# Kernel optimization log

Measured on AMD Instinct MI355X. Metric: run time of the kernel, lower is better.

The kernel has to match this reference:

```python
import jax, jax.numpy as jnp
import numpy as np

B, T, D = 64, 1024, 512      # batch, listener time, 2*listener_hidden
H = 512                      # speller_hidden_dim
M = 256                      # mlp_dim_in_attention
C = 63                       # output_class_dim
S = 64                       # max_label_len (decode steps)
INV_SQRT_2PI = 0.3989422804014327


def setup_inputs() -> dict:
    key = jax.random.key(0)
    ks = jax.random.split(key, 16)
    def lin(k, out_d, in_d, scale=1.0):
        return jax.random.normal(k, (out_d, in_d), jnp.float32) * (scale / np.sqrt(in_d))
    listener_feature = jax.random.normal(ks[0], (B, T, D), jnp.float32)
    labels = jax.random.randint(ks[1], (B, S), 0, C)
    ground_truth = jax.nn.one_hot(labels, C, dtype=jnp.float32)
    return {
        'listener_feature': listener_feature,
        'ground_truth': ground_truth,
        'phi_w': lin(ks[2], M, D, 0.5), 'phi_b': jnp.zeros((M,), jnp.float32),
        'psi_w': lin(ks[3], M, D, 0.5), 'psi_b': jnp.zeros((M,), jnp.float32),
        'w_ih0': lin(ks[4], 4 * H, C + H), 'w_hh0': lin(ks[5], 4 * H, H),
        'b_ih0': jnp.zeros((4 * H,), jnp.float32), 'b_hh0': jnp.zeros((4 * H,), jnp.float32),
        'w_ih1': lin(ks[6], 4 * H, H), 'w_hh1': lin(ks[7], 4 * H, H),
        'b_ih1': jnp.zeros((4 * H,), jnp.float32), 'b_hh1': jnp.zeros((4 * H,), jnp.float32),
        'char_w': lin(ks[8], C, 2 * H), 'char_b': jnp.zeros((C,), jnp.float32),
    }


def _lstm_cell(x, h, c, w_ih, w_hh, b_ih, b_hh):
    g = x @ w_ih.T + b_ih + h @ w_hh.T + b_hh
    i, f, gg, o = jnp.split(g, 4, axis=-1)  # torch gate order i,f,g,o
    c_new = jax.nn.sigmoid(f) * c + jax.nn.sigmoid(i) * jnp.tanh(gg)
    h_new = jax.nn.sigmoid(o) * jnp.tanh(c_new)
    return h_new, c_new


def _copula_score(energy):
    # energy: [B, T]. Gaussian marginal pdf * bivariate Gaussian copula density of
    # adjacent columns (columns 0 and T-1 keep copula factor 1, as in source loop).
    pdf = jnp.exp(-0.5 * energy * energy) * INV_SQRT_2PI
    a = energy[:, :-2]   # column i-1 for i in 1..T-2
    b = energy[:, 1:-1]  # column i
    am = a - a.mean(axis=0)
    bm = b - b.mean(axis=0)
    r = (am * bm).sum(axis=0) / jnp.sqrt((am * am).sum(axis=0) * (bm * bm).sum(axis=0) + 1e-12)
    det = 1.0 - r * r  # det of 2x2 correlation matrix
    det_s = jnp.maximum(det, 1e-6)
    quad = r * r * (a * a + b * b) - 2.0 * r * a * b
    cop = jnp.exp(-0.5 * quad / det_s) / jnp.sqrt(det_s)
    bad = (det < 0.01) | jnp.all(a == b, axis=0)
    cop = jnp.where(bad, 10.0, cop)
    coppdf = jnp.ones_like(energy).at[:, 1:-1].set(cop)
    ef1 = pdf * coppdf
    # source falls back to softmax(energy) if any column is all-zero (batch>3 here);
    # copula path goes through numpy in torch, i.e. it is detached from autograd.
    any_zero_col = jnp.any(jnp.all(energy == 0.0, axis=0))
    return jnp.where(any_zero_col,
                     jax.nn.softmax(energy, axis=-1),
                     jax.nn.softmax(jax.lax.stop_gradient(ef1), axis=-1))


def _speller(listener_feature, ground_truth, phi_w, phi_b, psi_w, psi_b,
             w_ih0, w_hh0, b_ih0, b_hh0, w_ih1, w_hh1, b_ih1, b_hh1,
             char_w, char_b):
    comp_listener = jax.nn.relu(jnp.einsum('btd,md->btm', listener_feature, psi_w) + psi_b)

    def step(carry, gt_t):
        h0, c0, h1, c1, rnn_in = carry
        h0, c0 = _lstm_cell(rnn_in, h0, c0, w_ih0, w_hh0, b_ih0, b_hh0)
        h1, c1 = _lstm_cell(h0, h1, c1, w_ih1, w_hh1, b_ih1, b_hh1)
        dec = h1  # [B, H] top-layer rnn_output
        comp_dec = jax.nn.relu(dec @ phi_w.T + phi_b)            # [B, M]
        energy = jnp.einsum('bm,btm->bt', comp_dec, comp_listener)
        att = _copula_score(energy)                              # [B, T]
        context = jnp.einsum('bt,btd->bd', att, listener_feature)
        concat = jnp.concatenate([dec, context], axis=-1)        # [B, 2H]
        raw_pred = jax.nn.log_softmax(concat @ char_w.T + char_b, axis=-1)
        new_in = jnp.concatenate([gt_t, context], axis=-1)       # teacher forcing
        return (h0, c0, h1, c1, new_in), (raw_pred, att)

    z = jnp.zeros((B, H), listener_feature.dtype)
    onehot0 = jnp.zeros((B, C), listener_feature.dtype).at[:, 0].set(1.0)
    init_in = jnp.concatenate([onehot0, listener_feature[:, 0, :]], axis=-1)
    gt_seq = jnp.transpose(ground_truth, (1, 0, 2))  # [S, B, C]
    _, (preds, atts) = jax.lax.scan(step, (z, z, z, z, init_in), gt_seq)
    return preds, atts  # [S,B,C] log-probs, [S,B,T] attention scores


def reference(listener_feature, ground_truth, phi_w, phi_b, psi_w, psi_b,
              w_ih0, w_hh0, b_ih0, b_hh0, w_ih1, w_hh1, b_ih1, b_hh1,
              char_w, char_b):
    return _speller(listener_feature, ground_truth, phi_w, phi_b, psi_w, psi_b,
                    w_ih0, w_hh0, b_ih0, b_hh0, w_ih1, w_hh1, b_ih1, b_hh1,
                    char_w, char_b)
```

## Files before the change

### kernel.cpp

```cpp
#include <hip/hip_runtime.h>
#include <hip/hip_bf16.h>
#include <math.h>

#define B_ 64
#define T_ 1024
#define D_ 512
#define H_ 512
#define M_ 256
#define CC 63
#define SS 64
#define INV_SQRT_2PI 0.3989422804014327f

typedef __attribute__((ext_vector_type(8))) short short8v;
typedef __attribute__((ext_vector_type(4))) float f32x4;

static __device__ __forceinline__ float bf2f(unsigned short u) {
    unsigned int x = ((unsigned int)u) << 16;
    return __uint_as_float(x);
}
static __device__ __forceinline__ unsigned short f2bf(float f) {
    unsigned int x = __float_as_uint(f);
    unsigned int r = (x + 0x7fff + ((x >> 16) & 1)) >> 16;
    return (unsigned short)r;
}
static __device__ __forceinline__ float sigm(float x) {
    return 1.f / (1.f + __expf(-x));
}
static __device__ __forceinline__ float wsum64(float v) {
    for (int o = 32; o > 0; o >>= 1) v += __shfl_xor(v, o, 64);
    return v;
}


__global__ __launch_bounds__(256) void k_conv(const float* __restrict__ src,
        unsigned short* __restrict__ dst, int n4) {
    int stride = gridDim.x * 256;
    for (int i = blockIdx.x * 256 + threadIdx.x; i < n4; i += stride) {
        float4 v = ((const float4*)src)[i];
        ushort4 o;
        o.x = f2bf(v.x); o.y = f2bf(v.y); o.z = f2bf(v.z); o.w = f2bf(v.w);
        ((ushort4*)dst)[i] = o;
    }
}

__global__ __launch_bounds__(256) void k_gemm_mfma(
        const unsigned short* __restrict__ Abf,
        const unsigned short* __restrict__ Bbf,
        const float* __restrict__ psib,
        unsigned short* __restrict__ clT) {
    __shared__ unsigned short As[64 * 40];
    __shared__ unsigned short Bs[64 * 40];
    __shared__ unsigned short Os[64 * 72];
    int tid = threadIdx.x;
    int p0 = (blockIdx.x >> 2) * 64;
    int m0 = (blockIdx.x & 3) * 64;
    int w = tid >> 6, l = tid & 63;
    int wp = (w & 1) * 32, wm = (w >> 1) * 32;
    f32x4 acc[2][2] = {};
    int srow = tid >> 2, sc = (tid & 3) * 8;
    for (int k0 = 0; k0 < 512; k0 += 32) {
        __syncthreads();
        *(short8v*)&As[srow * 40 + sc] = *(const short8v*)&Abf[(size_t)(p0 + srow) * 512 + k0 + sc];
        *(short8v*)&Bs[srow * 40 + sc] = *(const short8v*)&Bbf[(size_t)(m0 + srow) * 512 + k0 + sc];
        __syncthreads();
        int koff = (l >> 4) * 8;
        int rlo = l & 15;
        short8v a0 = *(short8v*)&As[(wp + rlo) * 40 + koff];
        short8v a1 = *(short8v*)&As[(wp + 16 + rlo) * 40 + koff];
        short8v b0 = *(short8v*)&Bs[(wm + rlo) * 40 + koff];
        short8v b1 = *(short8v*)&Bs[(wm + 16 + rlo) * 40 + koff];
        acc[0][0] = __builtin_amdgcn_mfma_f32_16x16x32_bf16(a0, b0, acc[0][0], 0, 0, 0);
        acc[0][1] = __builtin_amdgcn_mfma_f32_16x16x32_bf16(a0, b1, acc[0][1], 0, 0, 0);
        acc[1][0] = __builtin_amdgcn_mfma_f32_16x16x32_bf16(a1, b0, acc[1][0], 0, 0, 0);
        acc[1][1] = __builtin_amdgcn_mfma_f32_16x16x32_bf16(a1, b1, acc[1][1], 0, 0, 0);
    }
    __syncthreads();
#pragma unroll
    for (int pi = 0; pi < 2; ++pi)
#pragma unroll
        for (int mi = 0; mi < 2; ++mi)
#pragma unroll
            for (int r = 0; r < 4; ++r) {
                int tl = wp + pi * 16 + (l >> 4) * 4 + r;
                int ml = wm + mi * 16 + (l & 15);
                float v = fmaxf(acc[pi][mi][r] + psib[m0 + ml], 0.f);
                Os[ml * 72 + tl] = f2bf(v);
            }
    __syncthreads();
    int b = p0 >> 10, t0 = p0 & 1023;
    int mm = tid >> 2, c16 = (tid & 3) * 16;
    short8v v0 = *(short8v*)&Os[mm * 72 + c16];
    short8v v1 = *(short8v*)&Os[mm * 72 + c16 + 8];
    size_t base = ((size_t)(b * 256 + m0 + mm)) * 1024 + t0 + c16;
    *(short8v*)&clT[base] = v0;
    *(short8v*)&clT[base + 8] = v1;
}

__global__ __launch_bounds__(256) void k_init(const float* __restrict__ Lf,
        const float* __restrict__ gt,
        float* gtT, float* h0a, float* h1a, float* c0, float* c1,
        float* ctxT, float* ctxb) {
    int tid = threadIdx.x, blk = blockIdx.x;
    if (blk < 64) {
        for (int r = tid; r < CC * 64; r += 256) {
            int k = r >> 6, b = r & 63;
            gtT[blk * (CC * 64) + r] = gt[(b * SS + blk) * CC + k];
        }
    } else {
        int idx = (blk - 64) * 256 + tid;
        h0a[idx] = 0.f; h1a[idx] = 0.f; c0[idx] = 0.f; c1[idx] = 0.f;
        int d = idx >> 6, b = idx & 63;
        float v = Lf[(size_t)b * (T_ * D_) + d];
        ctxT[idx] = v;
        ctxb[b * 512 + d] = v;
    }
}


__global__ __launch_bounds__(256) void k_lstm0(
        int s, const float* __restrict__ gtT, const float* __restrict__ ctxT,
        const float* __restrict__ h0in, float* __restrict__ h0out,
        float* __restrict__ c0,
        const float* __restrict__ wih0, const float* __restrict__ whh0,
        const float* __restrict__ bih0, const float* __restrict__ bhh0,
        int* __restrict__ colZero,
        const float* __restrict__ h1bp, const float* __restrict__ ctxb,
        const float* __restrict__ charw, const float* __restrict__ charb,
        float* __restrict__ preds) {
    __shared__ float xs[4096];
    __shared__ float wsm[16 * 68];
    __shared__ float ex[16 * 64];
    __shared__ float lgs[64];
    int tid = threadIdx.x, uid = blockIdx.x;
    if (uid >= 128) {
        if (s > 0) {
            int b = uid - 128;
            float* cpx = xs;
            for (int i = tid; i < 1024; i += 256)
                cpx[i] = (i < 512) ? h1bp[b * 512 + i] : ctxb[b * 512 + (i - 512)];
            __syncthreads();
            int c = tid >> 2, kl = tid & 3;
            float p = 0.f;
            if (c < 63) {
                const float4* cw = (const float4*)&charw[(size_t)c * 1024 + kl * 256];
                const float4* cx = (const float4*)&cpx[kl * 256];
#pragma unroll
                for (int q = 0; q < 64; ++q) {
                    float4 w4 = cw[q], x4 = cx[q];
                    p = fmaf(x4.x, w4.x, p); p = fmaf(x4.y, w4.y, p);
                    p = fmaf(x4.z, w4.z, p); p = fmaf(x4.w, w4.w, p);
                }
            }
            p += __shfl_xor(p, 1, 64); p += __shfl_xor(p, 2, 64);
            if (kl == 0 && c < 63) lgs[c] = p + charb[c];
            if (tid == 0) lgs[63] = -1e30f;
            __syncthreads();
            if (tid < 64) {
                float lg = (tid < 63) ? lgs[tid] : -1e30f;
                float mx = lg;
                for (int o = 32; o > 0; o >>= 1) mx = fmaxf(mx, __shfl_xor(mx, o, 64));
                float ex2 = (tid < 63) ? __expf(lg - mx) : 0.f;
                float sume = wsum64(ex2);
                if (tid < 63)
                    preds[((size_t)(s - 1) * B_ + b) * CC + tid] = lg - mx - __logf(sume);
            }
        }
        return;
    }
    int r = tid >> 4, tb = tid & 15;
    float a0 = 0.f, a1 = 0.f, a2 = 0.f, a3 = 0.f;
    for (int kc = 0; kc < 17; ++kc) {
        int k0 = kc * 64;
        __syncthreads();
#pragma unroll
        for (int i = 0; i < 4; ++i) {
            int e4 = i * 256 + tid;
            int kk = e4 >> 4, b4 = (e4 & 15) * 4;
            int k = k0 + kk;
            float4 v;
            if (k < 63) {
                if (s > 0) v = *(const float4*)&gtT[(s - 1) * 4032 + k * 64 + b4];
                else { float o1 = (k == 0) ? 1.f : 0.f; v = make_float4(o1, o1, o1, o1); }
            } else if (k < 575)  v = *(const float4*)&ctxT[(k - 63) * 64 + b4];
            else if (k < 1087)   v = *(const float4*)&h0in[(k - 575) * 64 + b4];
            else                 v = make_float4(0.f, 0.f, 0.f, 0.f);
            *(float4*)&xs[kk * 64 + b4] = v;
        }
#pragma unroll
        for (int i = 0; i < 4; ++i) {
            int lidx = i * 256 + tid;
            int rr = lidx >> 6, kk = lidx & 63;
            int k = k0 + kk;
            int g2 = rr >> 2, uu = rr & 3;
            int jj = g2 * 512 + uid * 4 + uu;
            float wv;
            if (k < 575)       wv = wih0[(size_t)jj * 575 + k];
            else if (k < 1087) wv = whh0[(size_t)jj * 512 + (k - 575)];
            else               wv = 0.f;
            wsm[rr * 68 + kk] = wv;
        }
        __syncthreads();
        const float* wsr = &wsm[r * 68];
        const float* xsr = &xs[tb * 4];
#pragma unroll
        for (int kk = 0; kk < 64; ++kk) {
            float wv = wsr[kk];
            float4 x4 = *(const float4*)&xsr[kk * 64];
            a0 = fmaf(wv, x4.x, a0);
            a1 = fmaf(wv, x4.y, a1);
            a2 = fmaf(wv, x4.z, a2);
            a3 = fmaf(wv, x4.w, a3);
        }
    }
    {
        int g2 = r >> 2, uu = r & 3;
        int j = g2 * 512 + uid * 4 + uu;
        float bias = bih0[j] + bhh0[j];
        __syncthreads();
        *(float4*)&ex[r * 64 + tb * 4] =
            make_float4(a0 + bias, a1 + bias, a2 + bias, a3 + bias);
    }
    __syncthreads();
    {
        int ui = tid >> 6, b = tid & 63;
        float gi = ex[(0 * 4 + ui) * 64 + b];
        float gf = ex[(1 * 4 + ui) * 64 + b];
        float gg = ex[(2 * 4 + ui) * 64 + b];
        float go = ex[(3 * 4 + ui) * 64 + b];
        int u = uid * 4 + ui;
        float cv = c0[u * 64 + b];
        float cn = sigm(gf) * cv + sigm(gi) * tanhf(gg);
        float hn = sigm(go) * tanhf(cn);
        c0[u * 64 + b] = cn;
        h0out[u * 64 + b] = hn;
    }
    if (uid == 0) {
        for (int i = tid; i < 1024; i += 256) colZero[i] = 1;
    }
}

__global__ __launch_bounds__(256) void k_lstm1(
        const float* __restrict__ h0cur, const float* __restrict__ h1in,
        float* __restrict__ h1out, float* __restrict__ c1,
        float* __restrict__ h1bout,
        const float* __restrict__ wih1, const float* __restrict__ whh1,
        const float* __restrict__ bih1, const float* __restrict__ bhh1) {
    __shared__ float xs[4096];
    __shared__ float wsm[16 * 68];
    __shared__ float ex[16 * 64];
    int tid = threadIdx.x, uid = blockIdx.x;
    int r = tid >> 4, tb = tid & 15;
    float a0 = 0.f, a1 = 0.f, a2 = 0.f, a3 = 0.f;
    for (int kc = 0; kc < 16; ++kc) {
        int k0 = kc * 64;
        __syncthreads();
#pragma unroll
        for (int i = 0; i < 4; ++i) {
            int e4 = i * 256 + tid;
            int kk = e4 >> 4, b4 = (e4 & 15) * 4;
            int k = k0 + kk;
            float4 v = (k < 512) ? *(const float4*)&h0cur[k * 64 + b4]
                                 : *(const float4*)&h1in[(k - 512) * 64 + b4];
            *(float4*)&xs[kk * 64 + b4] = v;
        }
#pragma unroll
        for (int i = 0; i < 4; ++i) {
            int lidx = i * 256 + tid;
            int rr = lidx >> 6, kk = lidx & 63;
            int k = k0 + kk;
            int g2 = rr >> 2, uu = rr & 3;
            int jj = g2 * 512 + uid * 4 + uu;
            float wv = (k < 512) ? wih1[(size_t)jj * 512 + k]
                                 : whh1[(size_t)jj * 512 + (k - 512)];
            wsm[rr * 68 + kk] = wv;
        }
        __syncthreads();
        const float* wsr = &wsm[r * 68];
        const float* xsr = &xs[tb * 4];
#pragma unroll
        for (int kk = 0; kk < 64; ++kk) {
            float wv = wsr[kk];
            float4 x4 = *(const float4*)&xsr[kk * 64];
            a0 = fmaf(wv, x4.x, a0);
            a1 = fmaf(wv, x4.y, a1);
            a2 = fmaf(wv, x4.z, a2);
            a3 = fmaf(wv, x4.w, a3);
        }
    }
    {
        int g2 = r >> 2, uu = r & 3;
        int j = g2 * 512 + uid * 4 + uu;
        float bias = bih1[j] + bhh1[j];
        __syncthreads();
        *(float4*)&ex[r * 64 + tb * 4] =
            make_float4(a0 + bias, a1 + bias, a2 + bias, a3 + bias);
    }
    __syncthreads();
    {
        int ui = tid >> 6, b = tid & 63;
        float gi = ex[(0 * 4 + ui) * 64 + b];
        float gf = ex[(1 * 4 + ui) * 64 + b];
        float gg = ex[(2 * 4 + ui) * 64 + b];
        float go = ex[(3 * 4 + ui) * 64 + b];
        int u = uid * 4 + ui;
        float cv = c1[u * 64 + b];
        float cn = sigm(gf) * cv + sigm(gi) * tanhf(gg);
        float hn = sigm(go) * tanhf(cn);
        c1[u * 64 + b] = cn;
        h1out[u * 64 + b] = hn;
        h1bout[b * 512 + u] = hn;
    }
}

__global__ __launch_bounds__(256) void k_phi(
        const float* __restrict__ h1u,
        const float* __restrict__ phiw, const float* __restrict__ phib,
        float* __restrict__ cdb) {
    __shared__ float xs[4096];
    __shared__ float wsm[32 * 68];
    int tid = threadIdx.x;
    int m0 = blockIdx.x * 32;
    int mr = tid >> 3, bq = tid & 7;
    float bias = phib[m0 + mr];
    float acc[8] = {bias, bias, bias, bias, bias, bias, bias, bias};
    for (int kc = 0; kc < 8; ++kc) {
        int k0 = kc * 64;
        __syncthreads();
#pragma unroll
        for (int i = 0; i < 4; ++i) {
            int idx4 = i * 256 + tid;
            int kk = idx4 >> 4, b4 = (idx4 & 15) * 4;
            *(float4*)&xs[kk * 64 + b4] = *(const float4*)&h1u[(k0 + kk) * 64 + b4];
        }
#pragma unroll
        for (int i = 0; i < 2; ++i) {
            int idx4 = i * 256 + tid;
            int mm = idx4 >> 4, kk4 = (idx4 & 15) * 4;
            *(float4*)&wsm[mm * 68 + kk4] = *(const float4*)&phiw[(size_t)(m0 + mm) * 512 + k0 + kk4];
        }
        __syncthreads();
        const float* wr = &wsm[mr * 68];
#pragma unroll
        for (int kk = 0; kk < 64; ++kk) {
            float wv = wr[kk];
            const float* xp = &xs[kk * 64 + bq * 8];
#pragma unroll
            for (int j = 0; j < 8; ++j)
                acc[j] = fmaf(xp[j], wv, acc[j]);
        }
    }
#pragma unroll
    for (int j = 0; j < 8; ++j)
        cdb[(bq * 8 + j) * 256 + m0 + mr] = fmaxf(acc[j], 0.f);
}

__global__ __launch_bounds__(64) void k_energy(
        const float* __restrict__ cdb,
        const unsigned short* __restrict__ clT,
        float* __restrict__ energy_bt, float* __restrict__ energyT,
        int* __restrict__ colZero) {
    __shared__ float cdl[256];
    int tid = threadIdx.x;
    int b = blockIdx.x >> 1, half = blockIdx.x & 1;
#pragma unroll
    for (int j = 0; j < 4; ++j)
        cdl[j * 64 + tid] = cdb[b * 256 + j * 64 + tid];
    __syncthreads();
    int t8 = half * 512 + tid * 8;
    float e[8] = {0.f, 0.f, 0.f, 0.f, 0.f, 0.f, 0.f, 0.f};
    const unsigned short* base = clT + ((size_t)(b * 256)) * 1024 + t8;
#pragma unroll 8
    for (int m = 0; m < 256; ++m) {
        short8v v = *(const short8v*)(base + (size_t)m * 1024);
        float c = cdl[m];
        e[0] = fmaf(c, bf2f((unsigned short)v[0]), e[0]);
        e[1] = fmaf(c, bf2f((unsigned short)v[1]), e[1]);
        e[2] = fmaf(c, bf2f((unsigned short)v[2]), e[2]);
        e[3] = fmaf(c, bf2f((unsigned short)v[3]), e[3]);
        e[4] = fmaf(c, bf2f((unsigned short)v[4]), e[4]);
        e[5] = fmaf(c, bf2f((unsigned short)v[5]), e[5]);
        e[6] = fmaf(c, bf2f((unsigned short)v[6]), e[6]);
        e[7] = fmaf(c, bf2f((unsigned short)v[7]), e[7]);
    }
#pragma unroll
    for (int j = 0; j < 8; ++j) {
        int t = t8 + j;
        energyT[t * 64 + b] = e[j];
        if (e[j] != 0.f) colZero[t] = 0;
    }
    *(float4*)&energy_bt[b * 1024 + t8] = make_float4(e[0], e[1], e[2], e[3]);
    *(float4*)&energy_bt[b * 1024 + t8 + 4] = make_float4(e[4], e[5], e[6], e[7]);
}

__global__ __launch_bounds__(256) void k_cop(
        const float* __restrict__ energyT,
        float* __restrict__ rS, float* __restrict__ dsS, int* __restrict__ badS) {
    int tid = threadIdx.x;
    int wv = tid >> 6, b = tid & 63;
    int t = blockIdx.x * 4 + wv;
    if (t >= 1 && t < 1023) {
        float e = energyT[t * 64 + b];
        float a = energyT[(t - 1) * 64 + b];
        float ma = wsum64(a) * (1.f / 64.f);
        float mb = wsum64(e) * (1.f / 64.f);
        float am = a - ma, bm = e - mb;
        float sab = wsum64(am * bm);
        float saa = wsum64(am * am);
        float sbb = wsum64(bm * bm);
        int aeq = __all(a == e);
        float r = sab / sqrtf(saa * sbb + 1e-12f);
        float det = 1.f - r * r;
        int bad = (det < 0.01f || aeq) ? 1 : 0;
        float ds = fmaxf(det, 1e-6f);
        if (b == 0) { rS[t] = r; dsS[t] = ds; badS[t] = bad; }
    }
}

__global__ __launch_bounds__(256) void k_soft(
        int doSM, int s, int prow,
        const float* __restrict__ energy_bt, const int* __restrict__ colZero,
        const float* __restrict__ rS, const float* __restrict__ dsS,
        const int* __restrict__ badS,
        const float* __restrict__ h1bp, const float* __restrict__ ctxb,
        const float* __restrict__ charw, const float* __restrict__ charb,
        float* __restrict__ preds, float* __restrict__ atts,
        float* __restrict__ attbuf) {
    __shared__ float e_l[1024];
    __shared__ float red[256];
    __shared__ int zred[256];
    __shared__ float cpx[1024];
    __shared__ float lgs[64];
    int tid = threadIdx.x, b = blockIdx.x;
    if (doSM) {
        *(float4*)&e_l[tid * 4] = *(const float4*)&energy_bt[b * 1024 + tid * 4];
        int z = colZero[tid] | colZero[256 + tid] | colZero[512 + tid] | colZero[768 + tid];
        zred[tid] = z;
        __syncthreads();
        for (int o = 128; o > 0; o >>= 1) {
            if (tid < o) zred[tid] |= zred[tid + o];
            __syncthreads();
        }
        int zf = zred[0];
        float4 rv = *(const float4*)&rS[tid * 4];
        float4 dv = *(const float4*)&dsS[tid * 4];
        int4 bv = *(const int4*)&badS[tid * 4];
        float rvv[4] = {rv.x, rv.y, rv.z, rv.w};
        float dvv[4] = {dv.x, dv.y, dv.z, dv.w};
        int bvv[4] = {bv.x, bv.y, bv.z, bv.w};
        float vals[4];
#pragma unroll
        for (int i = 0; i < 4; ++i) {
            int t = tid * 4 + i;
            float e = e_l[t];
            if (zf) {
                vals[i] = e;
            } else {
                float cp;
                if (t == 0 || t == 1023) cp = 1.f;
                else if (bvv[i]) cp = 10.f;
                else {
                    float a = e_l[t - 1];
                    float r = rvv[i], ds = dvv[i];
                    float quad = r * r * (a * a + e * e) - 2.f * r * a * e;
                    cp = __expf(-0.5f * quad / ds) / sqrtf(ds);
                }
                vals[i] = __expf(-0.5f * e * e) * INV_SQRT_2PI * cp;
            }
        }
        float lm = fmaxf(fmaxf(vals[0], vals[1]), fmaxf(vals[2], vals[3]));
        red[tid] = lm;
        __syncthreads();
        for (int o = 128; o > 0; o >>= 1) {
            if (tid < o) red[tid] = fmaxf(red[tid], red[tid + o]);
            __syncthreads();
        }
        float M = red[0];
        __syncthreads();
        float e0 = __expf(vals[0] - M), e1 = __expf(vals[1] - M);
        float e2 = __expf(vals[2] - M), e3 = __expf(vals[3] - M);
        red[tid] = e0 + e1 + e2 + e3;
        __syncthreads();
        for (int o = 128; o > 0; o >>= 1) {
            if (tid < o) red[tid] += red[tid + o];
            __syncthreads();
        }
        float inv = 1.f / red[0];
        float4 a4 = make_float4(e0 * inv, e1 * inv, e2 * inv, e3 * inv);
        *(float4*)&attbuf[b * 1024 + tid * 4] = a4;
        *(float4*)&atts[((size_t)s * B_ + b) * 1024 + tid * 4] = a4;
    }
    if (prow >= 0) {
        __syncthreads();
        for (int i = tid; i < 1024; i += 256)
            cpx[i] = (i < 512) ? h1bp[b * 512 + i] : ctxb[b * 512 + (i - 512)];
        __syncthreads();
        int c = tid >> 2, kl = tid & 3;
        float p = 0.f;
        if (c < 63) {
            const float4* cw = (const float4*)&charw[(size_t)c * 1024 + kl * 256];
            const float4* cx = (const float4*)&cpx[kl * 256];
#pragma unroll
            for (int q = 0; q < 64; ++q) {
                float4 w4 = cw[q], x4 = cx[q];
                p = fmaf(x4.x, w4.x, p); p = fmaf(x4.y, w4.y, p);
                p = fmaf(x4.z, w4.z, p); p = fmaf(x4.w, w4.w, p);
            }
        }
        p += __shfl_xor(p, 1, 64); p += __shfl_xor(p, 2, 64);
        if (kl == 0 && c < 63) lgs[c] = p + charb[c];
        if (tid == 0) lgs[63] = -1e30f;
        __syncthreads();
        if (tid < 64) {
            float lg = (tid < 63) ? lgs[tid] : -1e30f;
            float mx = lg;
            for (int o = 32; o > 0; o >>= 1) mx = fmaxf(mx, __shfl_xor(mx, o, 64));
            float ex2 = (tid < 63) ? __expf(lg - mx) : 0.f;
            float sume = wsum64(ex2);
            if (tid < 63)
                preds[((size_t)prow * B_ + b) * CC + tid] = lg - mx - __logf(sume);
        }
    }
}

__global__ __launch_bounds__(256) void k_ctx(
        const float* __restrict__ attbuf, const unsigned short* __restrict__ Lbf,
        float* __restrict__ ctxT, float* __restrict__ ctxb) {
    __shared__ float att[1056];
    __shared__ float red2[256];
    int tid = threadIdx.x;
    int b = blockIdx.x >> 3, dq = blockIdx.x & 7, d0 = dq * 64;
    {
        float4 a4 = *(const float4*)&attbuf[b * 1024 + tid * 4];
        int t = tid * 4;
        int pk = t + (t >> 5);
        att[pk] = a4.x; att[pk + 1] = a4.y; att[pk + 2] = a4.z; att[pk + 3] = a4.w;
    }
    __syncthreads();
    int tc = tid >> 3, dg = tid & 7;
    const unsigned short* Lb = Lbf + (size_t)b * 524288 + (size_t)tc * 32 * 512 + d0 + dg * 8;
    float acc[8] = {0.f, 0.f, 0.f, 0.f, 0.f, 0.f, 0.f, 0.f};
#pragma unroll
    for (int i = 0; i < 32; ++i) {
        float wv = att[tc * 33 + i];
        short8v v = *(const short8v*)(Lb + (size_t)i * 512);
        acc[0] = fmaf(wv, bf2f((unsigned short)v[0]), acc[0]);
        acc[1] = fmaf(wv, bf2f((unsigned short)v[1]), acc[1]);
        acc[2] = fmaf(wv, bf2f((unsigned short)v[2]), acc[2]);
        acc[3] = fmaf(wv, bf2f((unsigned short)v[3]), acc[3]);
        acc[4] = fmaf(wv, bf2f((unsigned short)v[4]), acc[4]);
        acc[5] = fmaf(wv, bf2f((unsigned short)v[5]), acc[5]);
        acc[6] = fmaf(wv, bf2f((unsigned short)v[6]), acc[6]);
        acc[7] = fmaf(wv, bf2f((unsigned short)v[7]), acc[7]);
    }
#pragma unroll
    for (int j = 0; j < 8; ++j) {
        acc[j] += __shfl_xor(acc[j], 8, 64);
        acc[j] += __shfl_xor(acc[j], 16, 64);
        acc[j] += __shfl_xor(acc[j], 32, 64);
    }
    int w = tid >> 6;
    if ((tid & 56) == 0) {
#pragma unroll
        for (int j = 0; j < 8; ++j) red2[w * 64 + dg * 8 + j] = acc[j];
    }
    __syncthreads();
    if (tid < 64) {
        float cv = red2[tid] + red2[64 + tid] + red2[128 + tid] + red2[192 + tid];
        ctxT[(d0 + tid) * 64 + b] = cv;
        ctxb[b * 512 + d0 + tid] = cv;
    }
}

extern "C" void kernel_launch(void* const* d_in, const int* in_sizes, int n_in,
                              void* d_out, int out_size, void* d_ws, size_t ws_size,
                              hipStream_t stream) {
    const float* Lf   = (const float*)d_in[0];
    const float* gt   = (const float*)d_in[1];
    const float* phiw = (const float*)d_in[2];
    const float* phib = (const float*)d_in[3];
    const float* psiw = (const float*)d_in[4];
    const float* psib = (const float*)d_in[5];
    const float* wih0 = (const float*)d_in[6];
    const float* whh0 = (const float*)d_in[7];
    const float* bih0 = (const float*)d_in[8];
    const float* bhh0 = (const float*)d_in[9];
    const float* wih1 = (const float*)d_in[10];
    const float* whh1 = (const float*)d_in[11];
    const float* bih1 = (const float*)d_in[12];
    const float* bhh1 = (const float*)d_in[13];
    const float* charw = (const float*)d_in[14];
    const float* charb = (const float*)d_in[15];

    float* preds = (float*)d_out;
    float* atts  = (float*)d_out + (size_t)SS * B_ * CC;

    char* ws = (char*)d_ws;
    size_t off = 0;
    auto alloc = [&](size_t bytes) { size_t o = off; off = (off + bytes + 255) & ~(size_t)255; return o; };
    unsigned short* clT = (unsigned short*)(ws + alloc((size_t)B_ * M_ * T_ * 2));
    unsigned short* Lbf = (unsigned short*)(ws + alloc((size_t)B_ * T_ * D_ * 2));
    unsigned short* psibf = (unsigned short*)(ws + alloc((size_t)M_ * D_ * 2));
    float* gtT      = (float*)(ws + alloc((size_t)SS * CC * 64 * 4));
    float* h0p0     = (float*)(ws + alloc(H_ * B_ * 4));
    float* h0p1     = (float*)(ws + alloc(H_ * B_ * 4));
    float* h1p0     = (float*)(ws + alloc(H_ * B_ * 4));
    float* h1p1     = (float*)(ws + alloc(H_ * B_ * 4));
    float* hb0      = (float*)(ws + alloc(H_ * B_ * 4));
    float* hb1      = (float*)(ws + alloc(H_ * B_ * 4));
    float* c0       = (float*)(ws + alloc(H_ * B_ * 4));
    float* c1       = (float*)(ws + alloc(H_ * B_ * 4));
    float* ctxT     = (float*)(ws + alloc(H_ * B_ * 4));
    float* ctxb     = (float*)(ws + alloc(H_ * B_ * 4));
    float* cdb      = (float*)(ws + alloc(B_ * M_ * 4));
    float* energy_bt = (float*)(ws + alloc(B_ * T_ * 4));
    float* energyT   = (float*)(ws + alloc(B_ * T_ * 4));
    float* rS       = (float*)(ws + alloc(T_ * 4));
    float* dsS      = (float*)(ws + alloc(T_ * 4));
    int* badS       = (int*)(ws + alloc(T_ * 4));
    int* colZero    = (int*)(ws + alloc(T_ * 4));
    float* attbuf   = (float*)(ws + alloc(B_ * T_ * 4));

    k_conv<<<2048, 256, 0, stream>>>(Lf, Lbf, (B_ * T_ * D_) / 4);
    k_conv<<<128, 256, 0, stream>>>(psiw, psibf, (M_ * D_) / 4);
    k_gemm_mfma<<<4096, 256, 0, stream>>>(Lbf, psibf, psib, clT);
    k_init<<<192, 256, 0, stream>>>(Lf, gt, gtT, h0p0, h1p0, c0, c1, ctxT, ctxb);

    float* h0p[2] = {h0p0, h0p1};
    float* h1p[2] = {h1p0, h1p1};
    float* hb[2]  = {hb0, hb1};
    for (int s = 0; s < SS; ++s) {
        int pi = s & 1, po = pi ^ 1;
        k_lstm0<<<192, 256, 0, stream>>>(s, gtT, ctxT, h0p[pi], h0p[po], c0,
                                         wih0, whh0, bih0, bhh0, colZero,
                                         hb[po], ctxb, charw, charb, preds);
        k_lstm1<<<128, 256, 0, stream>>>(h0p[po], h1p[pi], h1p[po], c1, hb[pi],
                                         wih1, whh1, bih1, bhh1);
        k_phi<<<8, 256, 0, stream>>>(h1p[po], phiw, phib, cdb);
        k_energy<<<128, 64, 0, stream>>>(cdb, clT, energy_bt, energyT, colZero);
        k_cop<<<256, 256, 0, stream>>>(energyT, rS, dsS, badS);
        k_soft<<<64, 256, 0, stream>>>(1, s, -1, energy_bt, colZero, rS, dsS, badS,
                                       hb[po], ctxb, charw, charb,
                                       preds, atts, attbuf);
        k_ctx<<<512, 256, 0, stream>>>(attbuf, Lbf, ctxT, ctxb);
    }
    k_soft<<<64, 256, 0, stream>>>(0, SS - 1, SS - 1, energy_bt, colZero, rS, dsS, badS,
                                   hb[1], ctxb, charw, charb, preds, atts, attbuf);
}
```

Measured before the change: 8.803 ms.

## Fuse copula scoring into per-element values and merge softmax with context kernel

```diff
diff --git a/kernel.cpp b/kernel.cpp
--- a/kernel.cpp
+++ b/kernel.cpp
@@ -117,6 +117,40 @@
 }
 
 
+static __device__ __forceinline__ void charpred_body(int b, int prow, int tid,
+        const float* __restrict__ h1bp, const float* __restrict__ ctxb,
+        const float* __restrict__ charw, const float* __restrict__ charb,
+        float* __restrict__ preds, float* cpx, float* lgs) {
+    for (int i = tid; i < 1024; i += 256)
+        cpx[i] = (i < 512) ? h1bp[b * 512 + i] : ctxb[b * 512 + (i - 512)];
+    __syncthreads();
+    int c = tid >> 2, kl = tid & 3;
+    float p = 0.f;
+    if (c < 63) {
+        const float4* cw = (const float4*)&charw[(size_t)c * 1024 + kl * 256];
+        const float4* cx = (const float4*)&cpx[kl * 256];
+#pragma unroll
+        for (int q = 0; q < 64; ++q) {
+            float4 w4 = cw[q], x4 = cx[q];
+            p = fmaf(x4.x, w4.x, p); p = fmaf(x4.y, w4.y, p);
+            p = fmaf(x4.z, w4.z, p); p = fmaf(x4.w, w4.w, p);
+        }
+    }
+    p += __shfl_xor(p, 1, 64); p += __shfl_xor(p, 2, 64);
+    if (kl == 0 && c < 63) lgs[c] = p + charb[c];
+    if (tid == 0) lgs[63] = -1e30f;
+    __syncthreads();
+    if (tid < 64) {
+        float lg = (tid < 63) ? lgs[tid] : -1e30f;
+        float mx = lg;
+        for (int o = 32; o > 0; o >>= 1) mx = fmaxf(mx, __shfl_xor(mx, o, 64));
+        float ex2 = (tid < 63) ? __expf(lg - mx) : 0.f;
+        float sume = wsum64(ex2);
+        if (tid < 63)
+            preds[((size_t)prow * B_ + b) * CC + tid] = lg - mx - __logf(sume);
+    }
+}
+
 __global__ __launch_bounds__(256) void k_lstm0(
         int s, const float* __restrict__ gtT, const float* __restrict__ ctxT,
         const float* __restrict__ h0in, float* __restrict__ h0out,
@@ -133,38 +167,8 @@
     __shared__ float lgs[64];
     int tid = threadIdx.x, uid = blockIdx.x;
     if (uid >= 128) {
-        if (s > 0) {
-            int b = uid - 128;
-            float* cpx = xs;
-            for (int i = tid; i < 1024; i += 256)
-                cpx[i] = (i < 512) ? h1bp[b * 512 + i] : ctxb[b * 512 + (i - 512)];
-            __syncthreads();
-            int c = tid >> 2, kl = tid & 3;
-            float p = 0.f;
-            if (c < 63) {
-                const float4* cw = (const float4*)&charw[(size_t)c * 1024 + kl * 256];
-                const float4* cx = (const float4*)&cpx[kl * 256];
-#pragma unroll
-                for (int q = 0; q < 64; ++q) {
-                    float4 w4 = cw[q], x4 = cx[q];
-                    p = fmaf(x4.x, w4.x, p); p = fmaf(x4.y, w4.y, p);
-                    p = fmaf(x4.z, w4.z, p); p = fmaf(x4.w, w4.w, p);
-                }
-            }
-            p += __shfl_xor(p, 1, 64); p += __shfl_xor(p, 2, 64);
-            if (kl == 0 && c < 63) lgs[c] = p + charb[c];
-            if (tid == 0) lgs[63] = -1e30f;
-            __syncthreads();
-            if (tid < 64) {
-                float lg = (tid < 63) ? lgs[tid] : -1e30f;
-                float mx = lg;
-                for (int o = 32; o > 0; o >>= 1) mx = fmaxf(mx, __shfl_xor(mx, o, 64));
-                float ex2 = (tid < 63) ? __expf(lg - mx) : 0.f;
-                float sume = wsum64(ex2);
-                if (tid < 63)
-                    preds[((size_t)(s - 1) * B_ + b) * CC + tid] = lg - mx - __logf(sume);
-            }
-        }
+        if (s > 0)
+            charpred_body(uid - 128, s - 1, tid, h1bp, ctxb, charw, charb, preds, xs, lgs);
         return;
     }
     int r = tid >> 4, tb = tid & 15;
@@ -357,7 +361,7 @@
 __global__ __launch_bounds__(64) void k_energy(
         const float* __restrict__ cdb,
         const unsigned short* __restrict__ clT,
-        float* __restrict__ energy_bt, float* __restrict__ energyT,
+        float* __restrict__ energyT,
         int* __restrict__ colZero) {
     __shared__ float cdl[256];
     int tid = threadIdx.x;
@@ -388,153 +392,91 @@
         energyT[t * 64 + b] = e[j];
         if (e[j] != 0.f) colZero[t] = 0;
     }
-    *(float4*)&energy_bt[b * 1024 + t8] = make_float4(e[0], e[1], e[2], e[3]);
-    *(float4*)&energy_bt[b * 1024 + t8 + 4] = make_float4(e[4], e[5], e[6], e[7]);
-}
-
-__global__ __launch_bounds__(256) void k_cop(
-        const float* __restrict__ energyT,
-        float* __restrict__ rS, float* __restrict__ dsS, int* __restrict__ badS) {
+}
+
+__global__ __launch_bounds__(256) void k_copvals(
+        const float* __restrict__ energyT, const int* __restrict__ colZero,
+        float* __restrict__ vbuf) {
+    __shared__ int zred[256];
     int tid = threadIdx.x;
+    int z = colZero[tid] | colZero[256 + tid] | colZero[512 + tid] | colZero[768 + tid];
+    zred[tid] = z;
+    __syncthreads();
+    for (int o = 128; o > 0; o >>= 1) {
+        if (tid < o) zred[tid] |= zred[tid + o];
+        __syncthreads();
+    }
+    int zf = zred[0];
     int wv = tid >> 6, b = tid & 63;
     int t = blockIdx.x * 4 + wv;
-    if (t >= 1 && t < 1023) {
-        float e = energyT[t * 64 + b];
-        float a = energyT[(t - 1) * 64 + b];
-        float ma = wsum64(a) * (1.f / 64.f);
-        float mb = wsum64(e) * (1.f / 64.f);
-        float am = a - ma, bm = e - mb;
-        float sab = wsum64(am * bm);
-        float saa = wsum64(am * am);
-        float sbb = wsum64(bm * bm);
-        int aeq = __all(a == e);
-        float r = sab / sqrtf(saa * sbb + 1e-12f);
-        float det = 1.f - r * r;
-        int bad = (det < 0.01f || aeq) ? 1 : 0;
-        float ds = fmaxf(det, 1e-6f);
-        if (b == 0) { rS[t] = r; dsS[t] = ds; badS[t] = bad; }
-    }
-}
-
-__global__ __launch_bounds__(256) void k_soft(
-        int doSM, int s, int prow,
-        const float* __restrict__ energy_bt, const int* __restrict__ colZero,
-        const float* __restrict__ rS, const float* __restrict__ dsS,
-        const int* __restrict__ badS,
-        const float* __restrict__ h1bp, const float* __restrict__ ctxb,
-        const float* __restrict__ charw, const float* __restrict__ charb,
-        float* __restrict__ preds, float* __restrict__ atts,
-        float* __restrict__ attbuf) {
-    __shared__ float e_l[1024];
+    float e = energyT[t * 64 + b];
+    float val;
+    if (zf) {
+        val = e;
+    } else {
+        float cp;
+        if (t == 0 || t == 1023) {
+            cp = 1.f;
+        } else {
+            float a = energyT[(t - 1) * 64 + b];
+            float ma = wsum64(a) * (1.f / 64.f);
+            float mb = wsum64(e) * (1.f / 64.f);
+            float am = a - ma, bm = e - mb;
+            float sab = wsum64(am * bm);
+            float saa = wsum64(am * am);
+            float sbb = wsum64(bm * bm);
+            int aeq = __all(a == e);
+            float r = sab / sqrtf(saa * sbb + 1e-12f);
+            float det = 1.f - r * r;
+            if (det < 0.01f || aeq) cp = 10.f;
+            else {
+                float ds = fmaxf(det, 1e-6f);
+                float quad = r * r * (a * a + e * e) - 2.f * r * a * e;
+                cp = __expf(-0.5f * quad / ds) / sqrtf(ds);
+            }
+        }
+        val = __expf(-0.5f * e * e) * INV_SQRT_2PI * cp;
+    }
+    vbuf[b * 1024 + t] = val;
+}
+
+__global__ __launch_bounds__(256) void k_softctx(
+        int s, const float* __restrict__ vbuf,
+        const unsigned short* __restrict__ Lbf,
+        float* __restrict__ ctxT, float* __restrict__ ctxb,
+        float* __restrict__ atts) {
+    __shared__ float att[1056];
     __shared__ float red[256];
-    __shared__ int zred[256];
-    __shared__ float cpx[1024];
-    __shared__ float lgs[64];
-    int tid = threadIdx.x, b = blockIdx.x;
-    if (doSM) {
-        *(float4*)&e_l[tid * 4] = *(const float4*)&energy_bt[b * 1024 + tid * 4];
-        int z = colZero[tid] | colZero[256 + tid] | colZero[512 + tid] | colZero[768 + tid];
-        zred[tid] = z;
-        __syncthreads();
-        for (int o = 128; o > 0; o >>= 1) {
-            if (tid < o) zred[tid] |= zred[tid + o];
-            __syncthreads();
-        }
-        int zf = zred[0];
-        float4 rv = *(const float4*)&rS[tid * 4];
-        float4 dv = *(const float4*)&dsS[tid * 4];
-        int4 bv = *(const int4*)&badS[tid * 4];
-        float rvv[4] = {rv.x, rv.y, rv.z, rv.w};
-        float dvv[4] = {dv.x, dv.y, dv.z, dv.w};
-        int bvv[4] = {bv.x, bv.y, bv.z, bv.w};
-        float vals[4];
-#pragma unroll
-        for (int i = 0; i < 4; ++i) {
-            int t = tid * 4 + i;
-            float e = e_l[t];
-            if (zf) {
-                vals[i] = e;
-            } else {
-                float cp;
-                if (t == 0 || t == 1023) cp = 1.f;
-                else if (bvv[i]) cp = 10.f;
-                else {
-                    float a = e_l[t - 1];
-                    float r = rvv[i], ds = dvv[i];
-                    float quad = r * r * (a * a + e * e) - 2.f * r * a * e;
-                    cp = __expf(-0.5f * quad / ds) / sqrtf(ds);
-                }
-                vals[i] = __expf(-0.5f * e * e) * INV_SQRT_2PI * cp;
-            }
-        }
-        float lm = fmaxf(fmaxf(vals[0], vals[1]), fmaxf(vals[2], vals[3]));
-        red[tid] = lm;
-        __syncthreads();
-        for (int o = 128; o > 0; o >>= 1) {
-            if (tid < o) red[tid] = fmaxf(red[tid], red[tid + o]);
-            __syncthreads();
-        }
-        float M = red[0];
-        __syncthreads();
-        float e0 = __expf(vals[0] - M), e1 = __expf(vals[1] - M);
-        float e2 = __expf(vals[2] - M), e3 = __expf(vals[3] - M);
-        red[tid] = e0 + e1 + e2 + e3;
-        __syncthreads();
-        for (int o = 128; o > 0; o >>= 1) {
-            if (tid < o) red[tid] += red[tid + o];
-            __syncthreads();
-        }
-        float inv = 1.f / red[0];
-        float4 a4 = make_float4(e0 * inv, e1 * inv, e2 * inv, e3 * inv);
-        *(float4*)&attbuf[b * 1024 + tid * 4] = a4;
-        *(float4*)&atts[((size_t)s * B_ + b) * 1024 + tid * 4] = a4;
-    }
-    if (prow >= 0) {
-        __syncthreads();
-        for (int i = tid; i < 1024; i += 256)
-            cpx[i] = (i < 512) ? h1bp[b * 512 + i] : ctxb[b * 512 + (i - 512)];
-        __syncthreads();
-        int c = tid >> 2, kl = tid & 3;
-        float p = 0.f;
-        if (c < 63) {
-            const float4* cw = (const float4*)&charw[(size_t)c * 1024 + kl * 256];
-            const float4* cx = (const float4*)&cpx[kl * 256];
-#pragma unroll
-            for (int q = 0; q < 64; ++q) {
-                float4 w4 = cw[q], x4 = cx[q];
-                p = fmaf(x4.x, w4.x, p); p = fmaf(x4.y, w4.y, p);
-                p = fmaf(x4.z, w4.z, p); p = fmaf(x4.w, w4.w, p);
-            }
-        }
-        p += __shfl_xor(p, 1, 64); p += __shfl_xor(p, 2, 64);
-        if (kl == 0 && c < 63) lgs[c] = p + charb[c];
-        if (tid == 0) lgs[63] = -1e30f;
-        __syncthreads();
-        if (tid < 64) {
-            float lg = (tid < 63) ? lgs[tid] : -1e30f;
-            float mx = lg;
-            for (int o = 32; o > 0; o >>= 1) mx = fmaxf(mx, __shfl_xor(mx, o, 64));
-            float ex2 = (tid < 63) ? __expf(lg - mx) : 0.f;
-            float sume = wsum64(ex2);
-            if (tid < 63)
-                preds[((size_t)prow * B_ + b) * CC + tid] = lg - mx - __logf(sume);
-        }
-    }
-}
-
-__global__ __launch_bounds__(256) void k_ctx(
-        const float* __restrict__ attbuf, const unsigned short* __restrict__ Lbf,
-        float* __restrict__ ctxT, float* __restrict__ ctxb) {
-    __shared__ float att[1056];
     __shared__ float red2[256];
     int tid = threadIdx.x;
     int b = blockIdx.x >> 3, dq = blockIdx.x & 7, d0 = dq * 64;
+    float4 v4 = *(const float4*)&vbuf[b * 1024 + tid * 4];
+    float lm = fmaxf(fmaxf(v4.x, v4.y), fmaxf(v4.z, v4.w));
+    red[tid] = lm;
+    __syncthreads();
+    for (int o = 128; o > 0; o >>= 1) {
+        if (tid < o) red[tid] = fmaxf(red[tid], red[tid + o]);
+        __syncthreads();
+    }
+    float M = red[0];
+    __syncthreads();
+    float e0 = __expf(v4.x - M), e1 = __expf(v4.y - M);
+    float e2 = __expf(v4.z - M), e3 = __expf(v4.w - M);
+    red[tid] = e0 + e1 + e2 + e3;
+    __syncthreads();
+    for (int o = 128; o > 0; o >>= 1) {
+        if (tid < o) red[tid] += red[tid + o];
+        __syncthreads();
+    }
+    float inv = 1.f / red[0];
+    float4 a4 = make_float4(e0 * inv, e1 * inv, e2 * inv, e3 * inv);
     {
-        float4 a4 = *(const float4*)&attbuf[b * 1024 + tid * 4];
-        int t = tid * 4;
-        int pk = t + (t >> 5);
+        int t4 = tid * 4;
+        int pk = t4 + (t4 >> 5);
         att[pk] = a4.x; att[pk + 1] = a4.y; att[pk + 2] = a4.z; att[pk + 3] = a4.w;
     }
+    if (dq == 0)
+        *(float4*)&atts[((size_t)s * B_ + b) * 1024 + tid * 4] = a4;
     __syncthreads();
     int tc = tid >> 3, dg = tid & 7;
     const unsigned short* Lb = Lbf + (size_t)b * 524288 + (size_t)tc * 32 * 512 + d0 + dg * 8;
@@ -569,6 +511,16 @@
         ctxT[(d0 + tid) * 64 + b] = cv;
         ctxb[b * 512 + d0 + tid] = cv;
     }
+}
+
+__global__ __launch_bounds__(256) void k_charpred(
+        int prow,
+        const float* __restrict__ h1bp, const float* __restrict__ ctxb,
+        const float* __restrict__ charw, const float* __restrict__ charb,
+        float* __restrict__ preds) {
+    __shared__ float cpx[1024];
+    __shared__ float lgs[64];
+    charpred_body(blockIdx.x, prow, threadIdx.x, h1bp, ctxb, charw, charb, preds, cpx, lgs);
 }
 
 extern "C" void kernel_launch(void* const* d_in, const int* in_sizes, int n_in,
@@ -612,13 +564,9 @@
     float* ctxT     = (float*)(ws + alloc(H_ * B_ * 4));
     float* ctxb     = (float*)(ws + alloc(H_ * B_ * 4));
     float* cdb      = (float*)(ws + alloc(B_ * M_ * 4));
-    float* energy_bt = (float*)(ws + alloc(B_ * T_ * 4));
-    float* energyT   = (float*)(ws + alloc(B_ * T_ * 4));
-    float* rS       = (float*)(ws + alloc(T_ * 4));
-    float* dsS      = (float*)(ws + alloc(T_ * 4));
-    int* badS       = (int*)(ws + alloc(T_ * 4));
+    float* energyT  = (float*)(ws + alloc(B_ * T_ * 4));
+    float* vbuf     = (float*)(ws + alloc(B_ * T_ * 4));
     int* colZero    = (int*)(ws + alloc(T_ * 4));
-    float* attbuf   = (float*)(ws + alloc(B_ * T_ * 4));
 
     k_conv<<<2048, 256, 0, stream>>>(Lf, Lbf, (B_ * T_ * D_) / 4);
     k_conv<<<128, 256, 0, stream>>>(psiw, psibf, (M_ * D_) / 4);
@@ -636,13 +584,9 @@
         k_lstm1<<<128, 256, 0, stream>>>(h0p[po], h1p[pi], h1p[po], c1, hb[pi],
                                          wih1, whh1, bih1, bhh1);
         k_phi<<<8, 256, 0, stream>>>(h1p[po], phiw, phib, cdb);
-        k_energy<<<128, 64, 0, stream>>>(cdb, clT, energy_bt, energyT, colZero);
-        k_cop<<<256, 256, 0, stream>>>(energyT, rS, dsS, badS);
-        k_soft<<<64, 256, 0, stream>>>(1, s, -1, energy_bt, colZero, rS, dsS, badS,
-                                       hb[po], ctxb, charw, charb,
-                                       preds, atts, attbuf);
-        k_ctx<<<512, 256, 0, stream>>>(attbuf, Lbf, ctxT, ctxb);
-    }
-    k_soft<<<64, 256, 0, stream>>>(0, SS - 1, SS - 1, energy_bt, colZero, rS, dsS, badS,
-                                   hb[1], ctxb, charw, charb, preds, atts, attbuf);
-}
+        k_energy<<<128, 64, 0, stream>>>(cdb, clT, energyT, colZero);
+        k_copvals<<<256, 256, 0, stream>>>(energyT, colZero, vbuf);
+        k_softctx<<<512, 256, 0, stream>>>(s, vbuf, Lbf, ctxT, ctxb, atts);
+    }
+    k_charpred<<<64, 256, 0, stream>>>(SS - 1, hb[1], ctxb, charw, charb, preds);
+}
```

After: 9.146 ms. 1.04x slower.
